# Kernel optimization log

Hardware: AMD Instinct MI355X
Metric: run time of the kernel (lower is better)

Reference implementation:

```python
import jax, jax.numpy as jnp
import numpy as np

B, S, D, DK = 8, 2048, 768, 214
DROPOUT_P = 0.1


def setup_inputs() -> dict:
    key = jax.random.key(0)
    ks = jax.random.split(key, 11)
    x1 = jax.random.normal(ks[0], (B, S, D), jnp.float32)
    x2 = jax.random.normal(ks[1], (B, S, D), jnp.float32)
    x3 = jax.random.normal(ks[2], (B, S, D), jnp.float32)
    Wq = jax.random.normal(ks[3], (DK, D), jnp.float32) * (1.0 / np.sqrt(D))
    bq = jax.random.normal(ks[4], (DK,), jnp.float32) * 0.01
    Wk = jax.random.normal(ks[5], (DK, D), jnp.float32) * (1.0 / np.sqrt(D))
    bk = jax.random.normal(ks[6], (DK,), jnp.float32) * 0.01
    Wv = jax.random.normal(ks[7], (D, D), jnp.float32) * (1.0 / np.sqrt(D))
    bv = jax.random.normal(ks[8], (D,), jnp.float32) * 0.01
    # full-tensor elementwise divisor: uniform(0,1) + 1, as in the source
    inv_scale = jax.random.uniform(ks[9], (S, S), jnp.float32) + 1.0
    # deterministic inverted-dropout mask, keep prob = 1 - p
    keep = 1.0 - DROPOUT_P
    dropout_mask = (jax.random.uniform(ks[10], (B, S, S)) < keep).astype(jnp.float32) / keep
    return dict(x1=x1, x2=x2, x3=x3, Wq=Wq, bq=bq, Wk=Wk, bk=bk,
                Wv=Wv, bv=bv, inv_scale=inv_scale, dropout_mask=dropout_mask)


def reference(x1, x2, x3, Wq, bq, Wk, bk, Wv, bv, inv_scale, dropout_mask):
    q = jnp.einsum('bsd,kd->bsk', x1, Wq) + bq          # [B,S,DK]
    k = jnp.einsum('bsd,kd->bsk', x2, Wk) + bk          # [B,S,DK]
    v = jnp.einsum('bsd,ed->bse', x3, Wv) + bv          # [B,S,D]
    attn = jnp.einsum('bsk,btk->bst', q, k)             # [B,S,S]
    scaled = attn / inv_scale                           # elementwise full-tensor divisor
    p = jax.nn.softmax(scaled, axis=-1) * dropout_mask  # softmax + inverted dropout
    return jnp.einsum('bst,btd->bsd', p, v)             # [B,S,D]
```

## Files before the change

kernel.cpp:

```cpp
#include <hip/hip_runtime.h>
#include <hip/hip_bf16.h>

typedef unsigned short ushort;
typedef unsigned long long u64;
typedef short bf16x8 __attribute__((ext_vector_type(8)));
typedef _Float16 f16x8 __attribute__((ext_vector_type(8)));
typedef float f32x4 __attribute__((ext_vector_type(4)));

#define NB 8
#define SS 2048
#define DD 768
#define DKV 214
#define DKP 224
#define WROWS 256
#define MSHIFT 40.0f

__device__ __forceinline__ float bf2f(ushort u) {
  union { unsigned int i; float f; } v; v.i = ((unsigned int)u) << 16; return v.f;
}
__device__ __forceinline__ ushort f2bf(float f) {
  union { float f; unsigned int i; } v; v.f = f;
  unsigned int x = v.i;
  return (ushort)((x + 0x7fffu + ((x >> 16) & 1u)) >> 16);
}
__device__ __forceinline__ ushort f2h(float f) {
  union { _Float16 h; ushort u; } cv; cv.h = (_Float16)f; return cv.u;
}
__device__ __forceinline__ bf16x8 cvt8v(f32x4 a, f32x4 b) {
  bf16x8 r;
#pragma unroll
  for (int j = 0; j < 4; ++j) { r[j] = (short)f2bf(a[j]); r[j + 4] = (short)f2bf(b[j]); }
  return r;
}
__device__ __forceinline__ f16x8 cvt8h(f32x4 a, f32x4 b) {
  f16x8 r;
#pragma unroll
  for (int j = 0; j < 4; ++j) { r[j] = (_Float16)a[j]; r[j + 4] = (_Float16)b[j]; }
  return r;
}
__device__ __forceinline__ void gload16(const void* g, void* l) {
  __builtin_amdgcn_global_load_lds(
      (const __attribute__((address_space(1))) void*)g,
      (__attribute__((address_space(3))) void*)l, 16, 0, 0);
}

__global__ __launch_bounds__(256)
void prep_all(const float* __restrict__ dmk, const float* __restrict__ Wq,
              const float* __restrict__ Wk, const float* __restrict__ Wv,
              u64* __restrict__ dbits, ushort* __restrict__ Wqp,
              ushort* __restrict__ Wkp, ushort* __restrict__ Wvb,
              float* __restrict__ Z)
{
  const int tid0 = blockIdx.x * 256 + threadIdx.x;
  const int stride = gridDim.x * 256;
  for (int i = tid0; i < NB * SS; i += stride) Z[i] = 0.f;
  const int NW = WROWS * DD;
  const int NV = DD * DD;
  for (int i = tid0; i < 2 * NW + NV; i += stride) {
    if (i < NW) {
      int r = i / DD, c = i % DD;
      float v = (r < DKV) ? Wq[i] : 0.f;
      Wqp[(c >> 5) * (WROWS * 32) + r * 32 + (c & 31)] = f2h(v);
    } else if (i < 2 * NW) {
      int j = i - NW;
      int r = j / DD, c = j % DD;
      float v = (r < DKV) ? Wk[j] : 0.f;
      Wkp[(c >> 5) * (WROWS * 32) + r * 32 + (c & 31)] = f2h(v);
    } else {
      int j = i - 2 * NW;
      int r = j / DD, c = j % DD;
      Wvb[(c >> 5) * (DD * 32) + r * 32 + (c & 31)] = f2bf(Wv[j]);
    }
  }
  const int l = threadIdx.x & 63;
  const int wv = tid0 >> 6;
  const int nw = stride >> 6;
  const size_t nchunks = (size_t)NB * SS * SS / 256;
  for (size_t c = wv; c < nchunks; c += nw) {
    f32x4 v = *(const f32x4*)(dmk + c * 256 + 4 * l);
    u64 b0 = __ballot(v[0] > 0.5f);
    u64 b1 = __ballot(v[1] > 0.5f);
    u64 b2 = __ballot(v[2] > 0.5f);
    u64 b3 = __ballot(v[3] > 0.5f);
    if (l == 0) {
      u64* d = dbits + c * 4;
      d[0] = b0; d[1] = b1; d[2] = b2; d[3] = b3;
    }
  }
}

__global__ __launch_bounds__(256, 4)
void gemm_qk(const float* __restrict__ x1, const float* __restrict__ x2,
             const ushort* __restrict__ Wqp, const ushort* __restrict__ Wkp,
             const float* __restrict__ bq, const float* __restrict__ bk,
             ushort* __restrict__ Qp, ushort* __restrict__ Kp)
{
  const int m0 = blockIdx.x * 64;
  const int which = blockIdx.y;
  const int tid = threadIdx.x;
  const int w  = tid >> 6;
  const int l  = tid & 63;
  const int lr = l & 15;
  const int lh = l >> 4;

  const float*  A    = which ? x2 : x1;
  const ushort* Bw   = which ? Wkp : Wqp;
  const float*  bias = which ? bk : bq;
  ushort* Cp = which ? Kp : Qp;

  __shared__ __align__(16) char lds[2][256][64];

  const int srow = (w << 4) + (l >> 2);
  const size_t gc = (size_t)srow * 64 + (size_t)((((l & 3) ^ ((srow >> 1) & 3))) << 4);
  const char* gb = (const char*)Bw;

  const f32x4 fzero = {0.f, 0.f, 0.f, 0.f};
  f32x4 acc[14];
#pragma unroll
  for (int nt = 0; nt < 14; ++nt) acc[nt] = fzero;

  const float* arow = A + (size_t)(m0 + w * 16 + lr) * DD + lh * 8;

#define QKSTAGE(buf, kk) do {                                             \
    size_t ko = (size_t)(kk) * (WROWS * 64);                              \
    gload16(gb + ko + gc,         &lds[buf][w << 4][0]);                  \
    gload16(gb + ko + gc + 4096,  &lds[buf][(w << 4) + 64][0]);           \
    gload16(gb + ko + gc + 8192,  &lds[buf][(w << 4) + 128][0]);          \
    gload16(gb + ko + gc + 12288, &lds[buf][(w << 4) + 192][0]);          \
  } while (0)

  QKSTAGE(0, 0);
  f32x4 pa = *(const f32x4*)(arow);
  f32x4 pb = *(const f32x4*)(arow + 4);
  __syncthreads();

  for (int kk = 0; kk < 24; ++kk) {
    const int buf = kk & 1;
    if (kk < 23) QKSTAGE(buf ^ 1, kk + 1);
    f32x4 na = fzero, nb = fzero;
    if (kk < 23) {
      na = *(const f32x4*)(arow + (kk + 1) * 32);
      nb = *(const f32x4*)(arow + (kk + 1) * 32 + 4);
    }
    f16x8 af = cvt8h(pa, pb);
#pragma unroll
    for (int nt = 0; nt < 14; ++nt) {
      int br = nt * 16 + lr;
      int bo = (lh ^ ((br >> 1) & 3)) << 4;
      f16x8 wf = *(const f16x8*)&lds[buf][br][bo];
      acc[nt] = __builtin_amdgcn_mfma_f32_16x16x32_f16(af, wf, acc[nt], 0, 0, 0);
    }
    __syncthreads();
    pa = na; pb = nb;
  }
#undef QKSTAGE

#pragma unroll
  for (int nt = 0; nt < 14; ++nt) {
    int n = nt * 16 + lr;
    float bv = (n < DKV) ? bias[n] : 0.f;
#pragma unroll
    for (int r = 0; r < 4; ++r) {
      int m = m0 + w * 16 + lh * 4 + r;
      int bb = m >> 11, s = m & 2047;
      float val = (n < DKV) ? (acc[nt][r] + bv) : 0.f;
      Cp[((size_t)(bb * 7 + (n >> 5)) * SS + s) * 32 + (n & 31)] = f2h(val);
    }
  }
}

__global__ __launch_bounds__(256, 3)
void gemm_v(const float* __restrict__ A, const ushort* __restrict__ Bw,
            const float* __restrict__ bias, ushort* __restrict__ Vp)
{
  const int m0 = blockIdx.x * 64;
  const int n0 = blockIdx.y * 256;
  const int tid = threadIdx.x;
  const int w  = tid >> 6;
  const int l  = tid & 63;
  const int lr = l & 15;
  const int lh = l >> 4;

  __shared__ __align__(16) char smem[36864];
  typedef char VBuf[256][64];
  VBuf* stage = (VBuf*)smem;
  ushort (*lt)[72] = (ushort(*)[72])smem;

  const int srow = (w << 4) + (l >> 2);
  const size_t gc = (size_t)srow * 64 + (size_t)((((l & 3) ^ ((srow >> 1) & 3))) << 4);
  const char* gvw = (const char*)Bw + (size_t)n0 * 64;

  const f32x4 fzero = {0.f, 0.f, 0.f, 0.f};
  f32x4 acc[16];
#pragma unroll
  for (int nt = 0; nt < 16; ++nt) acc[nt] = fzero;

  const float* arow = A + (size_t)(m0 + w * 16 + lr) * DD + lh * 8;

#define VSTAGE(buf, kk) do {                                              \
    size_t ko = (size_t)(kk) * (DD * 64);                                 \
    gload16(gvw + ko + gc,         &stage[buf][w << 4][0]);               \
    gload16(gvw + ko + gc + 4096,  &stage[buf][(w << 4) + 64][0]);        \
    gload16(gvw + ko + gc + 8192,  &stage[buf][(w << 4) + 128][0]);       \
    gload16(gvw + ko + gc + 12288, &stage[buf][(w << 4) + 192][0]);       \
  } while (0)

  VSTAGE(0, 0);
  f32x4 pa = *(const f32x4*)(arow);
  f32x4 pb = *(const f32x4*)(arow + 4);
  __syncthreads();

  for (int kk = 0; kk < 24; ++kk) {
    const int buf = kk & 1;
    if (kk < 23) VSTAGE(buf ^ 1, kk + 1);
    f32x4 na = fzero, nb = fzero;
    if (kk < 23) {
      na = *(const f32x4*)(arow + (kk + 1) * 32);
      nb = *(const f32x4*)(arow + (kk + 1) * 32 + 4);
    }
    bf16x8 af = cvt8v(pa, pb);
#pragma unroll
    for (int nt = 0; nt < 16; ++nt) {
      int br = nt * 16 + lr;
      int bo = (lh ^ ((br >> 1) & 3)) << 4;
      bf16x8 bfr = *(const bf16x8*)&stage[buf][br][bo];
      acc[nt] = __builtin_amdgcn_mfma_f32_16x16x32_bf16(af, bfr, acc[nt], 0, 0, 0);
    }
    __syncthreads();
    pa = na; pb = nb;
  }
#undef VSTAGE

#pragma unroll
  for (int nt = 0; nt < 16; ++nt) {
    int nl = nt * 16 + lr;
    float bv = bias[n0 + nl];
#pragma unroll
    for (int r = 0; r < 4; ++r)
      lt[nl][w * 16 + lh * 4 + r] = f2bf(acc[nt][r] + bv);
  }
  __syncthreads();
  const int bb = m0 >> 11;
  const int s0 = m0 & 2047;
  for (int i = tid; i < 256 * 64; i += 256) {
    int nn = i >> 6, mm = i & 63;
    int d = n0 + nn, t = s0 + mm;
    Vp[((size_t)(bb * 64 + (t >> 5)) * DD + d) * 32 + (t & 31)] = lt[nn][mm];
  }
}

__global__ __launch_bounds__(512, 4)
void gemm_s(const ushort* __restrict__ Qp, const ushort* __restrict__ Kp,
            const float* __restrict__ isc, const u64* __restrict__ dbits,
            ushort* __restrict__ Pp, float* __restrict__ Z)
{
  const int bid = blockIdx.x;
  const int bb = bid & 7;
  const int tt = bid >> 3;
  const int m0 = (tt & 15) * 128;
  const int n0 = (tt >> 4) * 256;
  const int tid = threadIdx.x;
  const int w  = tid >> 6;
  const int l  = tid & 63;
  const int lr = l & 15;
  const int lh = l >> 4;
  const int wm = w & 1;
  const int wn = w >> 1;

  __shared__ __align__(16) char Qb[2][128][64];
  __shared__ __align__(16) char Kb[2][256][64];

  const int srow = (w << 4) + (l >> 2);
  const size_t gc = (size_t)srow * 64 + (size_t)((((l & 3) ^ ((srow >> 1) & 3))) << 4);

  const char* gq = (const char*)Qp + ((size_t)(bb * 7) * SS + m0) * 64;
  const char* gk = (const char*)Kp + ((size_t)(bb * 7) * SS + n0) * 64;

  const f32x4 fzero = {0.f, 0.f, 0.f, 0.f};
  f32x4 acc[4][4];
#pragma unroll
  for (int mf = 0; mf < 4; ++mf)
#pragma unroll
    for (int nf = 0; nf < 4; ++nf) acc[mf][nf] = fzero;

#define SSTAGE(buf, kk) do {                                            \
    size_t ko = (size_t)(kk) * (SS * 64);                               \
    gload16(gq + ko + gc,        &Qb[buf][w << 4][0]);                  \
    gload16(gk + ko + gc,        &Kb[buf][w << 4][0]);                  \
    gload16(gk + ko + gc + 8192, &Kb[buf][(w << 4) + 128][0]);          \
  } while (0)

  SSTAGE(0, 0);
  __syncthreads();
#pragma unroll 1
  for (int t = 0; t < 7; ++t) {
    const int buf = t & 1;
    if (t < 6) SSTAGE(buf ^ 1, t + 1);
    f16x8 bfr[4];
#pragma unroll
    for (int nf = 0; nf < 4; ++nf) {
      int br = wn * 64 + nf * 16 + lr;
      int bo = (lh ^ ((br >> 1) & 3)) << 4;
      bfr[nf] = *(const f16x8*)&Kb[buf][br][bo];
    }
#pragma unroll
    for (int mf = 0; mf < 4; ++mf) {
      int ar = wm * 64 + mf * 16 + lr;
      int ao = (lh ^ ((ar >> 1) & 3)) << 4;
      f16x8 af = *(const f16x8*)&Qb[buf][ar][ao];
#pragma unroll
      for (int nf = 0; nf < 4; ++nf)
        acc[mf][nf] = __builtin_amdgcn_mfma_f32_16x16x32_f16(af, bfr[nf], acc[mf][nf], 0, 0, 0);
    }
    __syncthreads();
  }
#undef SSTAGE

  const float KEEPR = 1.0f / 0.9f;
#pragma unroll
  for (int mf = 0; mf < 4; ++mf) {
#pragma unroll
    for (int r = 0; r < 4; ++r) {
      const int sr = m0 + wm * 64 + mf * 16 + lh * 4 + r;
      const u64 wbits = dbits[((size_t)bb * SS + sr) * 32 + (n0 >> 6) + (lr & 3)];
      float z = 0.f;
#pragma unroll
      for (int nf = 0; nf < 4; ++nf) {
        const int tc = n0 + wn * 64 + nf * 16 + lr;
        float iv = isc[(size_t)sr * SS + tc];
        float sval = acc[mf][nf][r] * __builtin_amdgcn_rcpf(iv);
        float e = __expf(sval - MSHIFT);
        z += e;
        float pm = ((wbits >> (wn * 16 + nf * 4 + (lr >> 2))) & 1ull) ? (e * KEEPR) : 0.f;
        Pp[((size_t)(bb * 64 + (tc >> 5)) * SS + sr) * 32 + (tc & 31)] = f2bf(pm);
      }
#pragma unroll
      for (int off = 1; off < 16; off <<= 1) z += __shfl_xor(z, off);
      if (lr == 0) atomicAdd(&Z[bb * SS + sr], z);
    }
  }
}

__global__ __launch_bounds__(256, 4)
void gemm_pv(const ushort* __restrict__ Pp, const ushort* __restrict__ Vp,
             const float* __restrict__ Z, float* __restrict__ out)
{
  const int bid = blockIdx.x;
  const int bb = bid & 7;
  const int tt = bid >> 3;
  const int m_idx = tt / 6;
  const int n_idx = tt - m_idx * 6;
  const int m0 = m_idx * 128;
  const int n0 = n_idx * 128;
  const int tid = threadIdx.x;
  const int w  = tid >> 6;
  const int l  = tid & 63;
  const int lr = l & 15;
  const int lh = l >> 4;
  const int wm = w & 1;
  const int wn = w >> 1;

  __shared__ __align__(16) char Plb[2][128][64];
  __shared__ __align__(16) char Vlb[2][128][64];

  const int srow = (w << 4) + (l >> 2);
  const size_t gc = (size_t)srow * 64 + (size_t)((((l & 3) ^ ((srow >> 1) & 3))) << 4);

  const char* gpb = (const char*)Pp + ((size_t)(bb * 64) * SS + m0) * 64;
  const char* gvb = (const char*)Vp + ((size_t)(bb * 64) * DD + n0) * 64;

  const f32x4 fzero = {0.f, 0.f, 0.f, 0.f};
  f32x4 acc[4][4];
#pragma unroll
  for (int mf = 0; mf < 4; ++mf)
#pragma unroll
    for (int nf = 0; nf < 4; ++nf) acc[mf][nf] = fzero;

#define PVSTAGE(t) do {                                                   \
    size_t k0 = (size_t)(t) * 2;                                          \
    gload16(gpb + k0 * (SS * 64) + gc,              &Plb[0][w << 4][0]);  \
    gload16(gpb + k0 * (SS * 64) + gc + 4096,       &Plb[0][(w << 4) + 64][0]); \
    gload16(gpb + (k0 + 1) * (SS * 64) + gc,        &Plb[1][w << 4][0]);  \
    gload16(gpb + (k0 + 1) * (SS * 64) + gc + 4096, &Plb[1][(w << 4) + 64][0]); \
    gload16(gvb + k0 * (DD * 64) + gc,              &Vlb[0][w << 4][0]);  \
    gload16(gvb + k0 * (DD * 64) + gc + 4096,       &Vlb[0][(w << 4) + 64][0]); \
    gload16(gvb + (k0 + 1) * (DD * 64) + gc,        &Vlb[1][w << 4][0]);  \
    gload16(gvb + (k0 + 1) * (DD * 64) + gc + 4096, &Vlb[1][(w << 4) + 64][0]); \
  } while (0)

  PVSTAGE(0);
  __syncthreads();
#pragma unroll 1
  for (int t = 0; t < 32; ++t) {
#pragma unroll
    for (int pk = 0; pk < 2; ++pk) {
      bf16x8 bfr[4];
#pragma unroll
      for (int nf = 0; nf < 4; ++nf) {
        int br = wn * 64 + nf * 16 + lr;
        int bo = (lh ^ ((br >> 1) & 3)) << 4;
        bfr[nf] = *(const bf16x8*)&Vlb[pk][br][bo];
      }
#pragma unroll
      for (int mf = 0; mf < 4; ++mf) {
        int ar = wm * 64 + mf * 16 + lr;
        int ao = (lh ^ ((ar >> 1) & 3)) << 4;
        bf16x8 af = *(const bf16x8*)&Plb[pk][ar][ao];
#pragma unroll
        for (int nf = 0; nf < 4; ++nf)
          acc[mf][nf] = __builtin_amdgcn_mfma_f32_16x16x32_bf16(af, bfr[nf], acc[mf][nf], 0, 0, 0);
      }
    }
    __syncthreads();
    if (t < 31) {
      PVSTAGE(t + 1);
      __syncthreads();
    }
  }
#undef PVSTAGE

#pragma unroll
  for (int mf = 0; mf < 4; ++mf) {
#pragma unroll
    for (int r = 0; r < 4; ++r) {
      const int sr = m0 + wm * 64 + mf * 16 + lh * 4 + r;
      float rz = __builtin_amdgcn_rcpf(Z[bb * SS + sr]);
#pragma unroll
      for (int nf = 0; nf < 4; ++nf) {
        const int dc = n0 + wn * 64 + nf * 16 + lr;
        out[((size_t)bb * SS + sr) * DD + dc] = acc[mf][nf][r] * rz;
      }
    }
  }
}

extern "C" void kernel_launch(void* const* d_in, const int* in_sizes, int n_in,
                              void* d_out, int out_size, void* d_ws, size_t ws_size,
                              hipStream_t stream) {
  const float* x1  = (const float*)d_in[0];
  const float* x2  = (const float*)d_in[1];
  const float* x3  = (const float*)d_in[2];
  const float* Wq  = (const float*)d_in[3];
  const float* bq  = (const float*)d_in[4];
  const float* Wk  = (const float*)d_in[5];
  const float* bk  = (const float*)d_in[6];
  const float* Wv  = (const float*)d_in[7];
  const float* bv  = (const float*)d_in[8];
  const float* isc = (const float*)d_in[9];
  const float* dmk = (const float*)d_in[10];
  float* out = (float*)d_out;

  const size_t QKN = (size_t)NB * 7 * SS * 32;
  const size_t VPN = (size_t)NB * 64 * DD * 32;
  const size_t WN  = (size_t)WROWS * DD;
  const size_t NV  = (size_t)DD * DD;
  const size_t PPN = (size_t)NB * 64 * SS * 32;

  ushort* Qp  = (ushort*)d_ws;
  ushort* Kp  = Qp + QKN;
  ushort* Vp  = Kp + QKN;
  ushort* Wqp = Vp + VPN;
  ushort* Wkp = Wqp + WN;
  ushort* Wvb = Wkp + WN;
  ushort* Pp  = Wvb + NV;
  float*  Zb  = (float*)(Pp + PPN);
  u64*    dbits = (u64*)(Zb + NB * SS);

  dim3 blk(256);
  prep_all<<<dim3(2048), blk, 0, stream>>>(dmk, Wq, Wk, Wv, dbits, Wqp, Wkp, Wvb, Zb);
  gemm_qk<<<dim3(256, 2), blk, 0, stream>>>(x1, x2, Wqp, Wkp, bq, bk, Qp, Kp);
  gemm_v <<<dim3(256, 3), blk, 0, stream>>>(x3, Wvb, bv, Vp);
  gemm_s <<<dim3(1024), dim3(512), 0, stream>>>(Qp, Kp, isc, dbits, Pp, Zb);
  gemm_pv<<<dim3(768),  dim3(256), 0, stream>>>(Pp, Vp, Zb, out);
}
```

Before: 237.2 us.

## Fuse Q/K/V projections and dropout bit-packing into one heterogeneous launch

Splits the prep kernel so only weight conversion and zeroing stay there. The Q/K GEMM, the V GEMM and the dropout-mask bitpacking now run as one kernel whose block index picks the role. The large mask read (about 128 MB of fp32) is meant to overlap with the compute-bound projection GEMMs instead of running serially before them. This also removes launch gaps. In exchange, the Q/K blocks now run at the occupancy hint of 3 instead of 4, and the memory-bound mask blocks compete with the GEMMs for bandwidth.

```diff
diff --git a/kernel.cpp b/kernel.cpp
--- a/kernel.cpp
+++ b/kernel.cpp
@@ -45,11 +45,10 @@
 }
 
 __global__ __launch_bounds__(256)
-void prep_all(const float* __restrict__ dmk, const float* __restrict__ Wq,
-              const float* __restrict__ Wk, const float* __restrict__ Wv,
-              u64* __restrict__ dbits, ushort* __restrict__ Wqp,
-              ushort* __restrict__ Wkp, ushort* __restrict__ Wvb,
-              float* __restrict__ Z)
+void prep_w(const float* __restrict__ Wq, const float* __restrict__ Wk,
+            const float* __restrict__ Wv, ushort* __restrict__ Wqp,
+            ushort* __restrict__ Wkp, ushort* __restrict__ Wvb,
+            float* __restrict__ Z)
 {
   const int tid0 = blockIdx.x * 256 + threadIdx.x;
   const int stride = gridDim.x * 256;
@@ -72,54 +71,67 @@
       Wvb[(c >> 5) * (DD * 32) + r * 32 + (c & 31)] = f2bf(Wv[j]);
     }
   }
-  const int l = threadIdx.x & 63;
-  const int wv = tid0 >> 6;
-  const int nw = stride >> 6;
-  const size_t nchunks = (size_t)NB * SS * SS / 256;
-  for (size_t c = wv; c < nchunks; c += nw) {
-    f32x4 v = *(const f32x4*)(dmk + c * 256 + 4 * l);
-    u64 b0 = __ballot(v[0] > 0.5f);
-    u64 b1 = __ballot(v[1] > 0.5f);
-    u64 b2 = __ballot(v[2] > 0.5f);
-    u64 b3 = __ballot(v[3] > 0.5f);
-    if (l == 0) {
-      u64* d = dbits + c * 4;
-      d[0] = b0; d[1] = b1; d[2] = b2; d[3] = b3;
-    }
-  }
-}
-
-__global__ __launch_bounds__(256, 4)
-void gemm_qk(const float* __restrict__ x1, const float* __restrict__ x2,
-             const ushort* __restrict__ Wqp, const ushort* __restrict__ Wkp,
-             const float* __restrict__ bq, const float* __restrict__ bk,
-             ushort* __restrict__ Qp, ushort* __restrict__ Kp)
+}
+
+__global__ __launch_bounds__(256, 3)
+void fused_proj(const float* __restrict__ x1, const float* __restrict__ x2,
+                const float* __restrict__ x3,
+                const ushort* __restrict__ Wqp, const ushort* __restrict__ Wkp,
+                const ushort* __restrict__ Wvb,
+                const float* __restrict__ bq, const float* __restrict__ bk,
+                const float* __restrict__ bv, const float* __restrict__ dmk,
+                ushort* __restrict__ Qp, ushort* __restrict__ Kp,
+                ushort* __restrict__ Vp, u64* __restrict__ dbits)
 {
-  const int m0 = blockIdx.x * 64;
-  const int which = blockIdx.y;
+  __shared__ __align__(16) char smem[36864];
+  const int bid = blockIdx.x;
   const int tid = threadIdx.x;
   const int w  = tid >> 6;
   const int l  = tid & 63;
   const int lr = l & 15;
   const int lh = l >> 4;
 
-  const float*  A    = which ? x2 : x1;
-  const ushort* Bw   = which ? Wkp : Wqp;
-  const float*  bias = which ? bk : bq;
-  ushort* Cp = which ? Kp : Qp;
-
-  __shared__ __align__(16) char lds[2][256][64];
+  if (bid >= 1280) {
+    const int db = bid - 1280;
+    const size_t wv = (size_t)db * 4 + w;
+    const size_t nw = 512 * 4;
+    const size_t nchunks = (size_t)NB * SS * SS / 256;
+    for (size_t c = wv; c < nchunks; c += nw) {
+      f32x4 v = *(const f32x4*)(dmk + c * 256 + 4 * l);
+      u64 b0 = __ballot(v[0] > 0.5f);
+      u64 b1 = __ballot(v[1] > 0.5f);
+      u64 b2 = __ballot(v[2] > 0.5f);
+      u64 b3 = __ballot(v[3] > 0.5f);
+      if (l == 0) {
+        u64* d = dbits + c * 4;
+        d[0] = b0; d[1] = b1; d[2] = b2; d[3] = b3;
+      }
+    }
+    return;
+  }
 
   const int srow = (w << 4) + (l >> 2);
   const size_t gc = (size_t)srow * 64 + (size_t)((((l & 3) ^ ((srow >> 1) & 3))) << 4);
-  const char* gb = (const char*)Bw;
-
   const f32x4 fzero = {0.f, 0.f, 0.f, 0.f};
-  f32x4 acc[14];
-#pragma unroll
-  for (int nt = 0; nt < 14; ++nt) acc[nt] = fzero;
-
-  const float* arow = A + (size_t)(m0 + w * 16 + lr) * DD + lh * 8;
+
+  if (bid >= 768) {
+    const int b2 = bid - 768;
+    const int m0 = (b2 & 255) * 64;
+    const int which = b2 >> 8;
+    const float*  A    = which ? x2 : x1;
+    const ushort* Bw   = which ? Wkp : Wqp;
+    const float*  bias = which ? bk : bq;
+    ushort* Cp = which ? Kp : Qp;
+
+    typedef char QBuf[256][64];
+    QBuf* lds = (QBuf*)smem;
+    const char* gb = (const char*)Bw;
+
+    f32x4 acc[14];
+#pragma unroll
+    for (int nt = 0; nt < 14; ++nt) acc[nt] = fzero;
+
+    const float* arow = A + (size_t)(m0 + w * 16 + lr) * DD + lh * 8;
 
 #define QKSTAGE(buf, kk) do {                                             \
     size_t ko = (size_t)(kk) * (WROWS * 64);                              \
@@ -129,73 +141,62 @@
     gload16(gb + ko + gc + 12288, &lds[buf][(w << 4) + 192][0]);          \
   } while (0)
 
-  QKSTAGE(0, 0);
-  f32x4 pa = *(const f32x4*)(arow);
-  f32x4 pb = *(const f32x4*)(arow + 4);
-  __syncthreads();
-
-  for (int kk = 0; kk < 24; ++kk) {
-    const int buf = kk & 1;
-    if (kk < 23) QKSTAGE(buf ^ 1, kk + 1);
-    f32x4 na = fzero, nb = fzero;
-    if (kk < 23) {
-      na = *(const f32x4*)(arow + (kk + 1) * 32);
-      nb = *(const f32x4*)(arow + (kk + 1) * 32 + 4);
-    }
-    f16x8 af = cvt8h(pa, pb);
+    QKSTAGE(0, 0);
+    f32x4 pa = *(const f32x4*)(arow);
+    f32x4 pb = *(const f32x4*)(arow + 4);
+    __syncthreads();
+
+    for (int kk = 0; kk < 24; ++kk) {
+      const int buf = kk & 1;
+      if (kk < 23) QKSTAGE(buf ^ 1, kk + 1);
+      f32x4 na = fzero, nb = fzero;
+      if (kk < 23) {
+        na = *(const f32x4*)(arow + (kk + 1) * 32);
+        nb = *(const f32x4*)(arow + (kk + 1) * 32 + 4);
+      }
+      f16x8 af = cvt8h(pa, pb);
+#pragma unroll
+      for (int nt = 0; nt < 14; ++nt) {
+        int br = nt * 16 + lr;
+        int bo = (lh ^ ((br >> 1) & 3)) << 4;
+        f16x8 wf = *(const f16x8*)&lds[buf][br][bo];
+        acc[nt] = __builtin_amdgcn_mfma_f32_16x16x32_f16(af, wf, acc[nt], 0, 0, 0);
+      }
+      __syncthreads();
+      pa = na; pb = nb;
+    }
+#undef QKSTAGE
+
 #pragma unroll
     for (int nt = 0; nt < 14; ++nt) {
-      int br = nt * 16 + lr;
-      int bo = (lh ^ ((br >> 1) & 3)) << 4;
-      f16x8 wf = *(const f16x8*)&lds[buf][br][bo];
-      acc[nt] = __builtin_amdgcn_mfma_f32_16x16x32_f16(af, wf, acc[nt], 0, 0, 0);
-    }
-    __syncthreads();
-    pa = na; pb = nb;
-  }
-#undef QKSTAGE
-
-#pragma unroll
-  for (int nt = 0; nt < 14; ++nt) {
-    int n = nt * 16 + lr;
-    float bv = (n < DKV) ? bias[n] : 0.f;
-#pragma unroll
-    for (int r = 0; r < 4; ++r) {
-      int m = m0 + w * 16 + lh * 4 + r;
-      int bb = m >> 11, s = m & 2047;
-      float val = (n < DKV) ? (acc[nt][r] + bv) : 0.f;
-      Cp[((size_t)(bb * 7 + (n >> 5)) * SS + s) * 32 + (n & 31)] = f2h(val);
-    }
-  }
-}
-
-__global__ __launch_bounds__(256, 3)
-void gemm_v(const float* __restrict__ A, const ushort* __restrict__ Bw,
-            const float* __restrict__ bias, ushort* __restrict__ Vp)
-{
-  const int m0 = blockIdx.x * 64;
-  const int n0 = blockIdx.y * 256;
-  const int tid = threadIdx.x;
-  const int w  = tid >> 6;
-  const int l  = tid & 63;
-  const int lr = l & 15;
-  const int lh = l >> 4;
-
-  __shared__ __align__(16) char smem[36864];
-  typedef char VBuf[256][64];
-  VBuf* stage = (VBuf*)smem;
-  ushort (*lt)[72] = (ushort(*)[72])smem;
-
-  const int srow = (w << 4) + (l >> 2);
-  const size_t gc = (size_t)srow * 64 + (size_t)((((l & 3) ^ ((srow >> 1) & 3))) << 4);
-  const char* gvw = (const char*)Bw + (size_t)n0 * 64;
-
-  const f32x4 fzero = {0.f, 0.f, 0.f, 0.f};
-  f32x4 acc[16];
-#pragma unroll
-  for (int nt = 0; nt < 16; ++nt) acc[nt] = fzero;
-
-  const float* arow = A + (size_t)(m0 + w * 16 + lr) * DD + lh * 8;
+      int n = nt * 16 + lr;
+      float bv2 = (n < DKV) ? bias[n] : 0.f;
+#pragma unroll
+      for (int r = 0; r < 4; ++r) {
+        int m = m0 + w * 16 + lh * 4 + r;
+        int bb = m >> 11, s = m & 2047;
+        float val = (n < DKV) ? (acc[nt][r] + bv2) : 0.f;
+        Cp[((size_t)(bb * 7 + (n >> 5)) * SS + s) * 32 + (n & 31)] = f2h(val);
+      }
+    }
+    return;
+  }
+
+  {
+    const int m0 = (bid & 255) * 64;
+    const int n0 = (bid >> 8) * 256;
+
+    typedef char VBuf[256][64];
+    VBuf* stage = (VBuf*)smem;
+    ushort (*lt)[72] = (ushort(*)[72])smem;
+
+    const char* gvw = (const char*)Wvb + (size_t)n0 * 64;
+
+    f32x4 acc[16];
+#pragma unroll
+    for (int nt = 0; nt < 16; ++nt) acc[nt] = fzero;
+
+    const float* arow = x3 + (size_t)(m0 + w * 16 + lr) * DD + lh * 8;
 
 #define VSTAGE(buf, kk) do {                                              \
     size_t ko = (size_t)(kk) * (DD * 64);                                 \
@@ -205,47 +206,48 @@
     gload16(gvw + ko + gc + 12288, &stage[buf][(w << 4) + 192][0]);       \
   } while (0)
 
-  VSTAGE(0, 0);
-  f32x4 pa = *(const f32x4*)(arow);
-  f32x4 pb = *(const f32x4*)(arow + 4);
-  __syncthreads();
-
-  for (int kk = 0; kk < 24; ++kk) {
-    const int buf = kk & 1;
-    if (kk < 23) VSTAGE(buf ^ 1, kk + 1);
-    f32x4 na = fzero, nb = fzero;
-    if (kk < 23) {
-      na = *(const f32x4*)(arow + (kk + 1) * 32);
-      nb = *(const f32x4*)(arow + (kk + 1) * 32 + 4);
-    }
-    bf16x8 af = cvt8v(pa, pb);
+    VSTAGE(0, 0);
+    f32x4 pa = *(const f32x4*)(arow);
+    f32x4 pb = *(const f32x4*)(arow + 4);
+    __syncthreads();
+
+    for (int kk = 0; kk < 24; ++kk) {
+      const int buf = kk & 1;
+      if (kk < 23) VSTAGE(buf ^ 1, kk + 1);
+      f32x4 na = fzero, nb = fzero;
+      if (kk < 23) {
+        na = *(const f32x4*)(arow + (kk + 1) * 32);
+        nb = *(const f32x4*)(arow + (kk + 1) * 32 + 4);
+      }
+      bf16x8 af = cvt8v(pa, pb);
+#pragma unroll
+      for (int nt = 0; nt < 16; ++nt) {
+        int br = nt * 16 + lr;
+        int bo = (lh ^ ((br >> 1) & 3)) << 4;
+        bf16x8 bfr = *(const bf16x8*)&stage[buf][br][bo];
+        acc[nt] = __builtin_amdgcn_mfma_f32_16x16x32_bf16(af, bfr, acc[nt], 0, 0, 0);
+      }
+      __syncthreads();
+      pa = na; pb = nb;
+    }
+#undef VSTAGE
+
 #pragma unroll
     for (int nt = 0; nt < 16; ++nt) {
-      int br = nt * 16 + lr;
-      int bo = (lh ^ ((br >> 1) & 3)) << 4;
-      bf16x8 bfr = *(const bf16x8*)&stage[buf][br][bo];
-      acc[nt] = __builtin_amdgcn_mfma_f32_16x16x32_bf16(af, bfr, acc[nt], 0, 0, 0);
+      int nl = nt * 16 + lr;
+      float bv2 = bv[n0 + nl];
+#pragma unroll
+      for (int r = 0; r < 4; ++r)
+        lt[nl][w * 16 + lh * 4 + r] = f2bf(acc[nt][r] + bv2);
     }
     __syncthreads();
-    pa = na; pb = nb;
-  }
-#undef VSTAGE
-
-#pragma unroll
-  for (int nt = 0; nt < 16; ++nt) {
-    int nl = nt * 16 + lr;
-    float bv = bias[n0 + nl];
-#pragma unroll
-    for (int r = 0; r < 4; ++r)
-      lt[nl][w * 16 + lh * 4 + r] = f2bf(acc[nt][r] + bv);
-  }
-  __syncthreads();
-  const int bb = m0 >> 11;
-  const int s0 = m0 & 2047;
-  for (int i = tid; i < 256 * 64; i += 256) {
-    int nn = i >> 6, mm = i & 63;
-    int d = n0 + nn, t = s0 + mm;
-    Vp[((size_t)(bb * 64 + (t >> 5)) * DD + d) * 32 + (t & 31)] = lt[nn][mm];
+    const int bb = m0 >> 11;
+    const int s0 = m0 & 2047;
+    for (int i = tid; i < 256 * 64; i += 256) {
+      int nn = i >> 6, mm = i & 63;
+      int d = n0 + nn, t = s0 + mm;
+      Vp[((size_t)(bb * 64 + (t >> 5)) * DD + d) * 32 + (t & 31)] = lt[nn][mm];
+    }
   }
 }
 
@@ -467,9 +469,9 @@
   u64*    dbits = (u64*)(Zb + NB * SS);
 
   dim3 blk(256);
-  prep_all<<<dim3(2048), blk, 0, stream>>>(dmk, Wq, Wk, Wv, dbits, Wqp, Wkp, Wvb, Zb);
-  gemm_qk<<<dim3(256, 2), blk, 0, stream>>>(x1, x2, Wqp, Wkp, bq, bk, Qp, Kp);
-  gemm_v <<<dim3(256, 3), blk, 0, stream>>>(x3, Wvb, bv, Vp);
+  prep_w<<<dim3(512), blk, 0, stream>>>(Wq, Wk, Wv, Wqp, Wkp, Wvb, Zb);
+  fused_proj<<<dim3(1792), blk, 0, stream>>>(x1, x2, x3, Wqp, Wkp, Wvb,
+                                             bq, bk, bv, dmk, Qp, Kp, Vp, dbits);
   gemm_s <<<dim3(1024), dim3(512), 0, stream>>>(Qp, Kp, isc, dbits, Pp, Zb);
   gemm_pv<<<dim3(768),  dim3(256), 0, stream>>>(Pp, Vp, Zb, out);
 }
```

Measured after the change: 245.1 us. 3.4% more time.
